# Kernel tuning notes

Hardware: AMD Instinct MI355X
Metric: run time of the kernel (lower is better)

Reference implementation:

```python
import jax, jax.numpy as jnp
import numpy as np

NUM_EXPERTS = 64
TOP_K = 2
DIM = 4096
TOKENS = 16384


def setup_inputs() -> dict:
    key = jax.random.key(0)
    k1, k2 = jax.random.split(key)
    x = jax.random.normal(k1, (TOKENS, DIM), dtype=jnp.float32)
    # nn.Linear weight: [num_experts, dim], scaled like kaiming-uniform-ish init
    w_gating = jax.random.normal(k2, (NUM_EXPERTS, DIM), dtype=jnp.float32) * (1.0 / np.sqrt(DIM))
    return {"x": x, "w_gating": w_gating}


def reference(x, w_gating):
    # gating linear (no bias, noise=0 / eval mode)
    logits = jnp.einsum("td,ed->te", x, w_gating)          # [tokens, experts]
    scores = jax.nn.softmax(logits, axis=-1)                # [tokens, experts]
    topk_scores, topk_experts = jax.lax.top_k(scores, TOP_K)  # [tokens, top_k]
    combine_weight = topk_scores
    me = scores.mean(axis=0)                                # [experts]
    ce = (scores > 0).astype(jnp.float32).mean(axis=0)      # [experts]
    load_balance_loss = (me * ce).sum() * NUM_EXPERTS
    z_loss = (jax.nn.logsumexp(logits, axis=-1) ** 2).mean()
    return topk_experts, combine_weight, scores, load_balance_loss, z_loss
```

## Files before the change

### kernel.cpp

```cpp
#include <hip/hip_runtime.h>
#include <hip/hip_bf16.h>

typedef __attribute__((ext_vector_type(8))) short bf16x8;
typedef __attribute__((ext_vector_type(4))) float f32x4;

#define N_TOKENS 16384
#define DIM 4096
#define TOKB 32
#define BK 128
#define NIT (DIM / BK)
#define NBUF 4
#define BUF_F (TOKB * BK)
#define N_EXP 64

#define OFF_W   (N_TOKENS * 2)
#define OFF_S   (N_TOKENS * 4)
#define OFF_LBL (N_TOKENS * 4 + N_TOKENS * N_EXP)
#define OFF_Z   (OFF_LBL + 1)

#define WS_WHI_F 512
#define WS_WLO_F (512 + (N_EXP * DIM) / 2)

typedef const __attribute__((address_space(1))) void GV;
typedef __attribute__((address_space(3))) void LV;

__device__ __forceinline__ unsigned int pkhi(float a, float b) {
  return __builtin_amdgcn_perm(__float_as_uint(b), __float_as_uint(a), 0x07060302u);
}
__device__ __forceinline__ float resid(float f) {
  return f - __uint_as_float(__float_as_uint(f) & 0xFFFF0000u);
}
__device__ __forceinline__ void tsplit8(const f32x4 p0, const f32x4 p1,
                                        bf16x8& hi, bf16x8& lo) {
  uint4 H = make_uint4(pkhi(p0[0], p0[1]), pkhi(p0[2], p0[3]),
                       pkhi(p1[0], p1[1]), pkhi(p1[2], p1[3]));
  float r0 = resid(p0[0]), r1 = resid(p0[1]), r2 = resid(p0[2]), r3 = resid(p0[3]);
  float r4 = resid(p1[0]), r5 = resid(p1[1]), r6 = resid(p1[2]), r7 = resid(p1[3]);
  uint4 L = make_uint4(pkhi(r0, r1), pkhi(r2, r3), pkhi(r4, r5), pkhi(r6, r7));
  hi = __builtin_bit_cast(bf16x8, H);
  lo = __builtin_bit_cast(bf16x8, L);
}

__global__ __launch_bounds__(256) void split_w_kernel(
    const float* __restrict__ w,
    unsigned short* __restrict__ whi, unsigned short* __restrict__ wlo)
{
  const int i = blockIdx.x * 256 + threadIdx.x;
  float f = w[i];
  unsigned short h = __builtin_bit_cast(unsigned short, __float2bfloat16(f));
  float hf = __uint_as_float(((unsigned)h) << 16);
  unsigned short l = __builtin_bit_cast(unsigned short, __float2bfloat16(f - hf));
  whi[i] = h;
  wlo[i] = l;
}

__global__ __launch_bounds__(512, 4) void router_kernel(
    const float* __restrict__ x,
    const unsigned short* __restrict__ whi, const unsigned short* __restrict__ wlo,
    float* __restrict__ out, float* __restrict__ ws)
{
  __shared__ __align__(16) float smem[NBUF * BUF_F];

  const int tid  = threadIdx.x;
  const int lane = tid & 63;
  const int wv   = __builtin_amdgcn_readfirstlane(tid >> 6);
  const int q    = wv & 1;
  const int kq   = wv >> 1;
  const int half = lane >> 4;
  const int r15  = lane & 15;
  const int tok0 = blockIdx.x * TOKB;

  const int row0 = wv * 4 + (lane >> 5);
  const int row1 = row0 + 2;
  const int sU   = lane & 31;
  const float* g0 = x + (size_t)(tok0 + row0) * DIM + ((sU ^ (row0 & 7)) << 2);
  const float* g1 = x + (size_t)(tok0 + row1) * DIM + ((sU ^ (row1 & 7)) << 2);
  float* const ldst = smem + wv * 512;

#define STAGE(buf, it_) do {                                                  \
    const float* s0_ = g0 + (size_t)(it_) * BK;                               \
    const float* s1_ = g1 + (size_t)(it_) * BK;                               \
    float* d_ = ldst + (buf) * BUF_F;                                         \
    __builtin_amdgcn_global_load_lds((GV*)s0_, (LV*)d_,       16, 0, 0);      \
    __builtin_amdgcn_global_load_lds((GV*)s1_, (LV*)(d_+256), 16, 0, 0);      \
  } while (0)

  const unsigned short* wh0 = whi + (size_t)(q * 32 + r15) * DIM + kq * 32 + half * 8;
  const unsigned short* wl0 = wlo + (size_t)(q * 32 + r15) * DIM + kq * 32 + half * 8;

  f32x4 acc[2][2];
#pragma unroll
  for (int tt = 0; tt < 2; ++tt)
#pragma unroll
    for (int n = 0; n < 2; ++n) acc[tt][n] = (f32x4){0.f, 0.f, 0.f, 0.f};

  STAGE(0, 0);
  bf16x8 cbh[2], cbl[2];
#pragma unroll
  for (int n = 0; n < 2; ++n) {
    cbh[n] = *(const bf16x8*)(wh0 + (size_t)n * 16 * DIM);
    cbl[n] = *(const bf16x8*)(wl0 + (size_t)n * 16 * DIM);
  }
  STAGE(1, 1);

  for (int it = 0; it < NIT; ++it) {
    const int cur = it & 3;
    const size_t kwn = (size_t)((it + 1 < NIT) ? it + 1 : NIT - 1) * BK;
    bf16x8 nbh[2], nbl[2];
#pragma unroll
    for (int n = 0; n < 2; ++n) {
      nbh[n] = *(const bf16x8*)(wh0 + kwn + (size_t)n * 16 * DIM);
      nbl[n] = *(const bf16x8*)(wl0 + kwn + (size_t)n * 16 * DIM);
    }
    STAGE((it + 2) & 3, (it + 2 < NIT) ? it + 2 : NIT - 1);

    asm volatile("s_waitcnt vmcnt(6)" ::: "memory");
    __builtin_amdgcn_s_barrier();

    const float* bufp = smem + cur * BUF_F;
#pragma unroll
    for (int tt = 0; tt < 2; ++tt) {
      const int rowA = tt * 16 + r15;
      const int g    = r15 & 7;
      const float* rp = bufp + rowA * BK;
      const int u0 = (kq * 8 + half * 2) ^ g;
      const int u1 = (kq * 8 + half * 2 + 1) ^ g;
      f32x4 p0 = *(const f32x4*)(rp + (u0 << 2));
      f32x4 p1 = *(const f32x4*)(rp + (u1 << 2));
      bf16x8 ah, al;
      tsplit8(p0, p1, ah, al);
#pragma unroll
      for (int n = 0; n < 2; ++n) {
        acc[tt][n] = __builtin_amdgcn_mfma_f32_16x16x32_bf16(ah, cbh[n], acc[tt][n], 0, 0, 0);
        acc[tt][n] = __builtin_amdgcn_mfma_f32_16x16x32_bf16(al, cbh[n], acc[tt][n], 0, 0, 0);
        acc[tt][n] = __builtin_amdgcn_mfma_f32_16x16x32_bf16(ah, cbl[n], acc[tt][n], 0, 0, 0);
      }
    }

#pragma unroll
    for (int n = 0; n < 2; ++n) { cbh[n] = nbh[n]; cbl[n] = nbl[n]; }
  }

  __syncthreads();

  float* lb = smem;
  {
    float* dst = lb + kq * (TOKB * 65);
#pragma unroll
    for (int tt = 0; tt < 2; ++tt) {
#pragma unroll
      for (int n = 0; n < 2; ++n) {
#pragma unroll
        for (int r = 0; r < 4; ++r) {
          dst[(tt * 16 + half * 4 + r) * 65 + q * 32 + n * 16 + r15] = acc[tt][n][r];
        }
      }
    }
  }
  __syncthreads();

  for (int i = tid; i < TOKB * 64; i += 512) {
    const int t = i >> 6, e = i & 63;
    lb[t * 65 + e] += lb[2080 + t * 65 + e] + lb[4160 + t * 65 + e] + lb[6240 + t * 65 + e];
  }
  __syncthreads();

  if (wv == 0 && lane < TOKB) {
    const int token = tok0 + lane;
    float v[64];
#pragma unroll
    for (int e = 0; e < 64; ++e) v[e] = lb[lane * 65 + e];
    float m = v[0];
#pragma unroll
    for (int e = 1; e < 64; ++e) m = fmaxf(m, v[e]);
    float sum = 0.f;
#pragma unroll
    for (int e = 0; e < 64; ++e) { v[e] = expf(v[e] - m); sum += v[e]; }
    const float inv = 1.0f / sum;
    float m1 = -1.f, m2 = -1.f;
    int   i1 = 0,    i2 = 0;
#pragma unroll
    for (int e = 0; e < 64; ++e) {
      float sc = v[e] * inv;
      lb[lane * 65 + e] = sc;
      if (sc > m1)      { m2 = m1; i2 = i1; m1 = sc; i1 = e; }
      else if (sc > m2) { m2 = sc; i2 = e; }
    }
    out[2 * token]         = (float)i1;
    out[2 * token + 1]     = (float)i2;
    out[OFF_W + 2 * token]     = m1;
    out[OFF_W + 2 * token + 1] = m2;

    float lse = m + logf(sum);
    float z = lse * lse;
#pragma unroll
    for (int off = 16; off > 0; off >>= 1) z += __shfl_down(z, off);
    if (lane == 0) atomicAdd(ws + 128, z);
  }
  __syncthreads();

  float* outS = out + OFF_S + (size_t)blockIdx.x * TOKB * 64;
  for (int i = tid; i < TOKB * 64; i += 512) {
    outS[i] = lb[(i >> 6) * 65 + (i & 63)];
  }

  if (wv == 0) {
    float sm = 0.f, cn = 0.f;
#pragma unroll
    for (int t = 0; t < TOKB; ++t) {
      float sc = lb[t * 65 + lane];
      sm += sc;
      cn += (sc > 0.f) ? 1.f : 0.f;
    }
    atomicAdd(ws + lane, sm);
    atomicAdd(ws + 64 + lane, cn);
  }
#undef STAGE
}

__global__ void finalize_kernel(const float* __restrict__ ws, float* __restrict__ out) {
  const int l = threadIdx.x;
  const float invT = 1.0f / (float)N_TOKENS;
  float me = ws[l] * invT;
  float ce = ws[64 + l] * invT;
  float p = me * ce;
#pragma unroll
  for (int off = 32; off > 0; off >>= 1) p += __shfl_down(p, off);
  if (l == 0) {
    out[OFF_LBL] = p * (float)N_EXP;
    out[OFF_Z]   = ws[128] * invT;
  }
}

extern "C" void kernel_launch(void* const* d_in, const int* in_sizes, int n_in,
                              void* d_out, int out_size, void* d_ws, size_t ws_size,
                              hipStream_t stream) {
  const float* x = (const float*)d_in[0];
  const float* w = (const float*)d_in[1];
  float* out = (float*)d_out;
  float* ws  = (float*)d_ws;
  unsigned short* whi = (unsigned short*)(ws + WS_WHI_F);
  unsigned short* wlo = (unsigned short*)(ws + WS_WLO_F);

  (void)hipMemsetAsync(d_ws, 0, 129 * sizeof(float), stream);
  split_w_kernel<<<(N_EXP * DIM) / 256, 256, 0, stream>>>(w, whi, wlo);
  router_kernel<<<N_TOKENS / TOKB, 512, 0, stream>>>(x, whi, wlo, out, ws);
  finalize_kernel<<<1, 64, 0, stream>>>(ws, out);
}
```

Before: 99.94 us.

## Split K across waves with per-wave LDS staging and separate epilogue kernel

The router kernel is restructured so each wave owns a 16-token by 1024-K slice. It stages that slice into its own double-buffered LDS region, which removes the block-wide barrier per K step, and computes all 64 experts per wave. Partial sums for the four K quarters go to a global workspace, and a new epilogue kernel reduces them and does the softmax, top-k and loss accumulation. This is meant to cut synchronisation stalls, but it adds a global round-trip of 4x16384x64 floats and an extra kernel launch.

```diff
diff --git a/kernel.cpp b/kernel.cpp
--- a/kernel.cpp
+++ b/kernel.cpp
@@ -6,11 +6,9 @@
 
 #define N_TOKENS 16384
 #define DIM 4096
-#define TOKB 32
-#define BK 128
-#define NIT (DIM / BK)
-#define NBUF 4
-#define BUF_F (TOKB * BK)
+#define KQ 1024
+#define CH 64
+#define NCH (KQ / CH)
 #define N_EXP 64
 
 #define OFF_W   (N_TOKENS * 2)
@@ -19,7 +17,8 @@
 #define OFF_Z   (OFF_LBL + 1)
 
 #define WS_WHI_F 512
-#define WS_WLO_F (512 + (N_EXP * DIM) / 2)
+#define WS_WLO_F (WS_WHI_F + (N_EXP * DIM) / 2)
+#define WS_PART_F (WS_WLO_F + (N_EXP * DIM) / 2)
 
 typedef const __attribute__((address_space(1))) void GV;
 typedef __attribute__((address_space(3))) void LV;
@@ -57,119 +56,137 @@
 __global__ __launch_bounds__(512, 4) void router_kernel(
     const float* __restrict__ x,
     const unsigned short* __restrict__ whi, const unsigned short* __restrict__ wlo,
-    float* __restrict__ out, float* __restrict__ ws)
+    float* __restrict__ part)
 {
-  __shared__ __align__(16) float smem[NBUF * BUF_F];
+  __shared__ __align__(16) float smem[8 * 2 * 16 * CH];
 
   const int tid  = threadIdx.x;
   const int lane = tid & 63;
   const int wv   = __builtin_amdgcn_readfirstlane(tid >> 6);
-  const int q    = wv & 1;
+  const int g    = wv & 1;
   const int kq   = wv >> 1;
   const int half = lane >> 4;
   const int r15  = lane & 15;
-  const int tok0 = blockIdx.x * TOKB;
-
-  const int row0 = wv * 4 + (lane >> 5);
-  const int row1 = row0 + 2;
-  const int sU   = lane & 31;
-  const float* g0 = x + (size_t)(tok0 + row0) * DIM + ((sU ^ (row0 & 7)) << 2);
-  const float* g1 = x + (size_t)(tok0 + row1) * DIM + ((sU ^ (row1 & 7)) << 2);
-  float* const ldst = smem + wv * 512;
-
-#define STAGE(buf, it_) do {                                                  \
-    const float* s0_ = g0 + (size_t)(it_) * BK;                               \
-    const float* s1_ = g1 + (size_t)(it_) * BK;                               \
-    float* d_ = ldst + (buf) * BUF_F;                                         \
-    __builtin_amdgcn_global_load_lds((GV*)s0_, (LV*)d_,       16, 0, 0);      \
-    __builtin_amdgcn_global_load_lds((GV*)s1_, (LV*)(d_+256), 16, 0, 0);      \
+  const int tok0 = blockIdx.x * 32 + g * 16;
+
+  float* const base = smem + wv * (2 * 16 * CH);
+
+  const int lrow = lane >> 4;
+  const int u    = lane & 15;
+  const float* gsrc[4];
+#pragma unroll
+  for (int i = 0; i < 4; ++i) {
+    const int row = 4 * i + lrow;
+    gsrc[i] = x + (size_t)(tok0 + row) * DIM + kq * KQ + ((u ^ (row & 7)) << 2);
+  }
+
+#define STAGE(bufsel, it_) do {                                                   \
+    float* dB_ = base + (bufsel) * (16 * CH);                                     \
+    __builtin_amdgcn_global_load_lds((GV*)(gsrc[0] + (size_t)(it_) * CH),         \
+                                     (LV*)(dB_ + 0 * 256), 16, 0, 0);             \
+    __builtin_amdgcn_global_load_lds((GV*)(gsrc[1] + (size_t)(it_) * CH),         \
+                                     (LV*)(dB_ + 1 * 256), 16, 0, 0);             \
+    __builtin_amdgcn_global_load_lds((GV*)(gsrc[2] + (size_t)(it_) * CH),         \
+                                     (LV*)(dB_ + 2 * 256), 16, 0, 0);             \
+    __builtin_amdgcn_global_load_lds((GV*)(gsrc[3] + (size_t)(it_) * CH),         \
+                                     (LV*)(dB_ + 3 * 256), 16, 0, 0);             \
   } while (0)
 
-  const unsigned short* wh0 = whi + (size_t)(q * 32 + r15) * DIM + kq * 32 + half * 8;
-  const unsigned short* wl0 = wlo + (size_t)(q * 32 + r15) * DIM + kq * 32 + half * 8;
-
-  f32x4 acc[2][2];
-#pragma unroll
-  for (int tt = 0; tt < 2; ++tt)
-#pragma unroll
-    for (int n = 0; n < 2; ++n) acc[tt][n] = (f32x4){0.f, 0.f, 0.f, 0.f};
+  const unsigned short* wh0 = whi + (size_t)r15 * DIM + kq * KQ + half * 8;
+  const unsigned short* wl0 = wlo + (size_t)r15 * DIM + kq * KQ + half * 8;
+
+  f32x4 acc[4];
+#pragma unroll
+  for (int n = 0; n < 4; ++n) acc[n] = (f32x4){0.f, 0.f, 0.f, 0.f};
 
   STAGE(0, 0);
-  bf16x8 cbh[2], cbl[2];
-#pragma unroll
-  for (int n = 0; n < 2; ++n) {
-    cbh[n] = *(const bf16x8*)(wh0 + (size_t)n * 16 * DIM);
-    cbl[n] = *(const bf16x8*)(wl0 + (size_t)n * 16 * DIM);
-  }
   STAGE(1, 1);
 
-  for (int it = 0; it < NIT; ++it) {
-    const int cur = it & 3;
-    const size_t kwn = (size_t)((it + 1 < NIT) ? it + 1 : NIT - 1) * BK;
-    bf16x8 nbh[2], nbl[2];
-#pragma unroll
-    for (int n = 0; n < 2; ++n) {
-      nbh[n] = *(const bf16x8*)(wh0 + kwn + (size_t)n * 16 * DIM);
-      nbl[n] = *(const bf16x8*)(wl0 + kwn + (size_t)n * 16 * DIM);
-    }
-    STAGE((it + 2) & 3, (it + 2 < NIT) ? it + 2 : NIT - 1);
-
-    asm volatile("s_waitcnt vmcnt(6)" ::: "memory");
-    __builtin_amdgcn_s_barrier();
-
-    const float* bufp = smem + cur * BUF_F;
-#pragma unroll
-    for (int tt = 0; tt < 2; ++tt) {
-      const int rowA = tt * 16 + r15;
-      const int g    = r15 & 7;
-      const float* rp = bufp + rowA * BK;
-      const int u0 = (kq * 8 + half * 2) ^ g;
-      const int u1 = (kq * 8 + half * 2 + 1) ^ g;
-      f32x4 p0 = *(const f32x4*)(rp + (u0 << 2));
-      f32x4 p1 = *(const f32x4*)(rp + (u1 << 2));
+  for (int it = 0; it < NCH; ++it) {
+    const float* bufp = base + (it & 1) * (16 * CH);
+    const int g8 = r15 & 7;
+    const float* rp = bufp + r15 * CH;
+
+    bf16x8 bh[4], bl[4];
+#pragma unroll
+    for (int n = 0; n < 4; ++n) {
+      const size_t o = (size_t)it * CH + (size_t)n * 16 * DIM;
+      bh[n] = *(const bf16x8*)(wh0 + o);
+      bl[n] = *(const bf16x8*)(wl0 + o);
+    }
+    asm volatile("s_waitcnt vmcnt(12)" ::: "memory");
+    {
+      const int b0 = (half * 2) ^ g8, b1 = (half * 2 + 1) ^ g8;
+      f32x4 p0 = *(const f32x4*)(rp + (b0 << 2));
+      f32x4 p1 = *(const f32x4*)(rp + (b1 << 2));
       bf16x8 ah, al;
       tsplit8(p0, p1, ah, al);
 #pragma unroll
-      for (int n = 0; n < 2; ++n) {
-        acc[tt][n] = __builtin_amdgcn_mfma_f32_16x16x32_bf16(ah, cbh[n], acc[tt][n], 0, 0, 0);
-        acc[tt][n] = __builtin_amdgcn_mfma_f32_16x16x32_bf16(al, cbh[n], acc[tt][n], 0, 0, 0);
-        acc[tt][n] = __builtin_amdgcn_mfma_f32_16x16x32_bf16(ah, cbl[n], acc[tt][n], 0, 0, 0);
+      for (int n = 0; n < 4; ++n) {
+        acc[n] = __builtin_amdgcn_mfma_f32_16x16x32_bf16(ah, bh[n], acc[n], 0, 0, 0);
+        acc[n] = __builtin_amdgcn_mfma_f32_16x16x32_bf16(al, bh[n], acc[n], 0, 0, 0);
+        acc[n] = __builtin_amdgcn_mfma_f32_16x16x32_bf16(ah, bl[n], acc[n], 0, 0, 0);
       }
     }
 
 #pragma unroll
-    for (int n = 0; n < 2; ++n) { cbh[n] = nbh[n]; cbl[n] = nbl[n]; }
-  }
-
+    for (int n = 0; n < 4; ++n) {
+      const size_t o = (size_t)it * CH + 32 + (size_t)n * 16 * DIM;
+      bh[n] = *(const bf16x8*)(wh0 + o);
+      bl[n] = *(const bf16x8*)(wl0 + o);
+    }
+    {
+      const int b0 = (8 + half * 2) ^ g8, b1 = (8 + half * 2 + 1) ^ g8;
+      f32x4 p0 = *(const f32x4*)(rp + (b0 << 2));
+      f32x4 p1 = *(const f32x4*)(rp + (b1 << 2));
+      bf16x8 ah, al;
+      tsplit8(p0, p1, ah, al);
+#pragma unroll
+      for (int n = 0; n < 4; ++n) {
+        acc[n] = __builtin_amdgcn_mfma_f32_16x16x32_bf16(ah, bh[n], acc[n], 0, 0, 0);
+        acc[n] = __builtin_amdgcn_mfma_f32_16x16x32_bf16(al, bh[n], acc[n], 0, 0, 0);
+        acc[n] = __builtin_amdgcn_mfma_f32_16x16x32_bf16(ah, bl[n], acc[n], 0, 0, 0);
+      }
+    }
+
+    asm volatile("s_waitcnt lgkmcnt(0)" ::: "memory");
+    STAGE(it & 1, (it + 2 < NCH) ? it + 2 : NCH - 1);
+  }
+
+#pragma unroll
+  for (int n = 0; n < 4; ++n) {
+#pragma unroll
+    for (int r = 0; r < 4; ++r) {
+      part[((size_t)kq * N_TOKENS + tok0 + half * 4 + r) * 64 + n * 16 + r15] = acc[n][r];
+    }
+  }
+#undef STAGE
+}
+
+__global__ __launch_bounds__(256) void epilogue_kernel(
+    const float* __restrict__ part, float* __restrict__ out, float* __restrict__ ws)
+{
+  __shared__ float lds[64 * 65];
+  const int tid  = threadIdx.x;
+  const int lane = tid & 63;
+  const int wv   = tid >> 6;
+  const int tok0 = blockIdx.x * 64;
+
+  for (int i = tid; i < 64 * 64; i += 256) {
+    const int t = i >> 6, e = i & 63;
+    const size_t idx = (size_t)(tok0 + t) * 64 + e;
+    lds[t * 65 + e] = part[idx]
+                    + part[(size_t)N_TOKENS * 64 + idx]
+                    + part[(size_t)2 * N_TOKENS * 64 + idx]
+                    + part[(size_t)3 * N_TOKENS * 64 + idx];
+  }
   __syncthreads();
 
-  float* lb = smem;
-  {
-    float* dst = lb + kq * (TOKB * 65);
-#pragma unroll
-    for (int tt = 0; tt < 2; ++tt) {
-#pragma unroll
-      for (int n = 0; n < 2; ++n) {
-#pragma unroll
-        for (int r = 0; r < 4; ++r) {
-          dst[(tt * 16 + half * 4 + r) * 65 + q * 32 + n * 16 + r15] = acc[tt][n][r];
-        }
-      }
-    }
-  }
-  __syncthreads();
-
-  for (int i = tid; i < TOKB * 64; i += 512) {
-    const int t = i >> 6, e = i & 63;
-    lb[t * 65 + e] += lb[2080 + t * 65 + e] + lb[4160 + t * 65 + e] + lb[6240 + t * 65 + e];
-  }
-  __syncthreads();
-
-  if (wv == 0 && lane < TOKB) {
+  if (wv == 0) {
     const int token = tok0 + lane;
     float v[64];
 #pragma unroll
-    for (int e = 0; e < 64; ++e) v[e] = lb[lane * 65 + e];
+    for (int e = 0; e < 64; ++e) v[e] = lds[lane * 65 + e];
     float m = v[0];
 #pragma unroll
     for (int e = 1; e < 64; ++e) m = fmaxf(m, v[e]);
@@ -182,40 +199,39 @@
 #pragma unroll
     for (int e = 0; e < 64; ++e) {
       float sc = v[e] * inv;
-      lb[lane * 65 + e] = sc;
+      lds[lane * 65 + e] = sc;
       if (sc > m1)      { m2 = m1; i2 = i1; m1 = sc; i1 = e; }
       else if (sc > m2) { m2 = sc; i2 = e; }
     }
-    out[2 * token]         = (float)i1;
-    out[2 * token + 1]     = (float)i2;
+    out[2 * token]             = (float)i1;
+    out[2 * token + 1]         = (float)i2;
     out[OFF_W + 2 * token]     = m1;
     out[OFF_W + 2 * token + 1] = m2;
 
     float lse = m + logf(sum);
     float z = lse * lse;
 #pragma unroll
-    for (int off = 16; off > 0; off >>= 1) z += __shfl_down(z, off);
+    for (int off = 32; off > 0; off >>= 1) z += __shfl_down(z, off);
     if (lane == 0) atomicAdd(ws + 128, z);
   }
   __syncthreads();
 
-  float* outS = out + OFF_S + (size_t)blockIdx.x * TOKB * 64;
-  for (int i = tid; i < TOKB * 64; i += 512) {
-    outS[i] = lb[(i >> 6) * 65 + (i & 63)];
+  float* outS = out + OFF_S + (size_t)blockIdx.x * 64 * 64;
+  for (int i = tid; i < 64 * 64; i += 256) {
+    outS[i] = lds[(i >> 6) * 65 + (i & 63)];
   }
 
   if (wv == 0) {
     float sm = 0.f, cn = 0.f;
 #pragma unroll
-    for (int t = 0; t < TOKB; ++t) {
-      float sc = lb[t * 65 + lane];
+    for (int t = 0; t < 64; ++t) {
+      float sc = lds[t * 65 + lane];
       sm += sc;
       cn += (sc > 0.f) ? 1.f : 0.f;
     }
     atomicAdd(ws + lane, sm);
     atomicAdd(ws + 64 + lane, cn);
   }
-#undef STAGE
 }
 
 __global__ void finalize_kernel(const float* __restrict__ ws, float* __restrict__ out) {
@@ -241,9 +257,11 @@
   float* ws  = (float*)d_ws;
   unsigned short* whi = (unsigned short*)(ws + WS_WHI_F);
   unsigned short* wlo = (unsigned short*)(ws + WS_WLO_F);
+  float* part = ws + WS_PART_F;
 
   (void)hipMemsetAsync(d_ws, 0, 129 * sizeof(float), stream);
   split_w_kernel<<<(N_EXP * DIM) / 256, 256, 0, stream>>>(w, whi, wlo);
-  router_kernel<<<N_TOKENS / TOKB, 512, 0, stream>>>(x, whi, wlo, out, ws);
+  router_kernel<<<N_TOKENS / 32, 512, 0, stream>>>(x, whi, wlo, part);
+  epilogue_kernel<<<N_TOKENS / 64, 256, 0, stream>>>(part, out, ws);
   finalize_kernel<<<1, 64, 0, stream>>>(ws, out);
 }
```

Measured after the change: 171.5 us. 1.72x slower.

## Pre-permute split bf16 gating weights into per-wave fragment order for contiguous loads

Applied to the files above, without the earlier changes.

The weight split kernel now writes the hi/lo bf16 halves in a layout ordered by (kq, q, iteration, n, lane), so each wave's B fragments for one K-step form a contiguous 1 KB block. This replaces strided per-row 16-byte loads across 16 expert rows with fully coalesced loads. The register prefetch of the next step's weights is dropped: weights are loaded at the start of each iteration and covered only by the barrier wait, with vmcnt raised to 8 to match. The swizzle index for the x tile is also rewritten, and exposing weight-load latency inside the loop is a risk.

```diff
diff --git a/kernel.cpp b/kernel.cpp
--- a/kernel.cpp
+++ b/kernel.cpp
@@ -46,12 +46,17 @@
     unsigned short* __restrict__ whi, unsigned short* __restrict__ wlo)
 {
   const int i = blockIdx.x * 256 + threadIdx.x;
+  const int e = i >> 12, k = i & 4095;
   float f = w[i];
   unsigned short h = __builtin_bit_cast(unsigned short, __float2bfloat16(f));
   float hf = __uint_as_float(((unsigned)h) << 16);
   unsigned short l = __builtin_bit_cast(unsigned short, __float2bfloat16(f - hf));
-  whi[i] = h;
-  wlo[i] = l;
+  const int q = e >> 5, n = (e >> 4) & 1, r15 = e & 15;
+  const int it = k >> 7, kq = (k >> 5) & 3, half = (k >> 3) & 3, j = k & 7;
+  const int lane = half * 16 + r15;
+  const int idx = (((kq * 2 + q) * 32 + it) * 1024) + n * 512 + lane * 8 + j;
+  whi[idx] = h;
+  wlo[idx] = l;
 }
 
 __global__ __launch_bounds__(512, 4) void router_kernel(
@@ -85,8 +90,9 @@
     __builtin_amdgcn_global_load_lds((GV*)s1_, (LV*)(d_+256), 16, 0, 0);      \
   } while (0)
 
-  const unsigned short* wh0 = whi + (size_t)(q * 32 + r15) * DIM + kq * 32 + half * 8;
-  const unsigned short* wl0 = wlo + (size_t)(q * 32 + r15) * DIM + kq * 32 + half * 8;
+  const unsigned short* wph = whi + ((kq * 2 + q) << 15);
+  const unsigned short* wpl = wlo + ((kq * 2 + q) << 15);
+  const int lo16 = lane * 8;
 
   f32x4 acc[2][2];
 #pragma unroll
@@ -95,26 +101,19 @@
     for (int n = 0; n < 2; ++n) acc[tt][n] = (f32x4){0.f, 0.f, 0.f, 0.f};
 
   STAGE(0, 0);
-  bf16x8 cbh[2], cbl[2];
-#pragma unroll
-  for (int n = 0; n < 2; ++n) {
-    cbh[n] = *(const bf16x8*)(wh0 + (size_t)n * 16 * DIM);
-    cbl[n] = *(const bf16x8*)(wl0 + (size_t)n * 16 * DIM);
-  }
   STAGE(1, 1);
 
   for (int it = 0; it < NIT; ++it) {
     const int cur = it & 3;
-    const size_t kwn = (size_t)((it + 1 < NIT) ? it + 1 : NIT - 1) * BK;
-    bf16x8 nbh[2], nbl[2];
-#pragma unroll
-    for (int n = 0; n < 2; ++n) {
-      nbh[n] = *(const bf16x8*)(wh0 + kwn + (size_t)n * 16 * DIM);
-      nbl[n] = *(const bf16x8*)(wl0 + kwn + (size_t)n * 16 * DIM);
-    }
+    const unsigned short* ph = wph + it * 1024;
+    const unsigned short* pl = wpl + it * 1024;
+    bf16x8 bh0 = *(const bf16x8*)(ph + lo16);
+    bf16x8 bh1 = *(const bf16x8*)(ph + 512 + lo16);
+    bf16x8 bl0 = *(const bf16x8*)(pl + lo16);
+    bf16x8 bl1 = *(const bf16x8*)(pl + 512 + lo16);
     STAGE((it + 2) & 3, (it + 2 < NIT) ? it + 2 : NIT - 1);
 
-    asm volatile("s_waitcnt vmcnt(6)" ::: "memory");
+    asm volatile("s_waitcnt vmcnt(8)" ::: "memory");
     __builtin_amdgcn_s_barrier();
 
     const float* bufp = smem + cur * BUF_F;
@@ -123,24 +122,22 @@
       const int rowA = tt * 16 + r15;
       const int g    = r15 & 7;
       const float* rp = bufp + rowA * BK;
-      const int u0 = (kq * 8 + half * 2) ^ g;
-      const int u1 = (kq * 8 + half * 2 + 1) ^ g;
+      const int u0 = kq * 8 + ((half * 2) ^ g);
+      const int u1 = kq * 8 + ((half * 2 + 1) ^ g);
       f32x4 p0 = *(const f32x4*)(rp + (u0 << 2));
       f32x4 p1 = *(const f32x4*)(rp + (u1 << 2));
       bf16x8 ah, al;
       tsplit8(p0, p1, ah, al);
-#pragma unroll
-      for (int n = 0; n < 2; ++n) {
-        acc[tt][n] = __builtin_amdgcn_mfma_f32_16x16x32_bf16(ah, cbh[n], acc[tt][n], 0, 0, 0);
-        acc[tt][n] = __builtin_amdgcn_mfma_f32_16x16x32_bf16(al, cbh[n], acc[tt][n], 0, 0, 0);
-        acc[tt][n] = __builtin_amdgcn_mfma_f32_16x16x32_bf16(ah, cbl[n], acc[tt][n], 0, 0, 0);
-      }
-    }
-
-#pragma unroll
-    for (int n = 0; n < 2; ++n) { cbh[n] = nbh[n]; cbl[n] = nbl[n]; }
-  }
-
+      acc[tt][0] = __builtin_amdgcn_mfma_f32_16x16x32_bf16(ah, bh0, acc[tt][0], 0, 0, 0);
+      acc[tt][0] = __builtin_amdgcn_mfma_f32_16x16x32_bf16(al, bh0, acc[tt][0], 0, 0, 0);
+      acc[tt][0] = __builtin_amdgcn_mfma_f32_16x16x32_bf16(ah, bl0, acc[tt][0], 0, 0, 0);
+      acc[tt][1] = __builtin_amdgcn_mfma_f32_16x16x32_bf16(ah, bh1, acc[tt][1], 0, 0, 0);
+      acc[tt][1] = __builtin_amdgcn_mfma_f32_16x16x32_bf16(al, bh1, acc[tt][1], 0, 0, 0);
+      acc[tt][1] = __builtin_amdgcn_mfma_f32_16x16x32_bf16(ah, bl1, acc[tt][1], 0, 0, 0);
+    }
+  }
+
+  asm volatile("s_waitcnt vmcnt(0)" ::: "memory");
   __syncthreads();
 
   float* lb = smem;
```

New measurement: 81.49 us. 1.23x faster.
